# Kernel optimization log

Measured on AMD Instinct MI355X. Metric: run time of the kernel, lower is better.

Reference implementation:

```python
import jax, jax.numpy as jnp
import numpy as np

N = 100000   # nodes
E = 800000   # edges
D = 64       # hidden_channels
H = 4        # heads
C = D        # out_channels per head (PyG: out_channels=hidden)


def setup_inputs() -> dict:
    key = jax.random.key(0)
    ks = jax.random.split(key, 20)
    inp = {}
    inp['x'] = jax.random.normal(ks[0], (N, D), dtype=jnp.float32)
    inp['edge_index'] = jax.random.randint(ks[1], (2, E), 0, N, dtype=jnp.int32)
    i = 2
    for layer in (1, 2):
        for nm in ('Wq', 'Wk', 'Wv'):
            inp[f'{nm}{layer}'] = jax.random.normal(ks[i], (D, H * C), dtype=jnp.float32) * 0.05; i += 1
            inp[f'b{nm[1]}{layer}'] = jnp.zeros((H * C,), dtype=jnp.float32)
        inp[f'Ws{layer}'] = jax.random.normal(ks[i], (D, D), dtype=jnp.float32) * 0.05; i += 1
        inp[f'bs{layer}'] = jnp.zeros((D,), dtype=jnp.float32)
    return inp


def _transformer_conv(x, src, dst, Wq, bq, Wk, bk, Wv, bv, Ws, bs):
    n = x.shape[0]
    q = (x @ Wq + bq).reshape(n, H, C)
    k = (x @ Wk + bk).reshape(n, H, C)
    v = (x @ Wv + bv).reshape(n, H, C)
    # per-edge attention logits: [E, H]
    alpha = jnp.einsum('ehc,ehc->eh', q[dst], k[src]) / np.sqrt(C).astype(np.float32)
    # segment softmax over incoming edges of each destination node
    amax = jax.ops.segment_max(alpha, dst, num_segments=n)          # [N, H]
    ex = jnp.exp(alpha - amax[dst])                                 # [E, H]
    denom = jax.ops.segment_sum(ex, dst, num_segments=n)           # [N, H]
    attn = ex / (denom[dst] + 1e-16)                                # [E, H]
    msg = v[src] * attn[:, :, None]                                 # [E, H, C]
    agg = jax.ops.segment_sum(msg, dst, num_segments=n)            # [N, H, C]
    # concat=False -> mean over heads; root_weight skip connection
    return agg.mean(axis=1) + x @ Ws + bs


def reference(x, edge_index, Wq1, bq1, Wk1, bk1, Wv1, bv1, Ws1, bs1,
              Wq2, bq2, Wk2, bk2, Wv2, bv2, Ws2, bs2):
    src, dst = edge_index[0], edge_index[1]
    h = _transformer_conv(x, src, dst, Wq1, bq1, Wk1, bk1, Wv1, bv1, Ws1, bs1)
    h = jax.nn.relu(h)
    out = _transformer_conv(h, src, dst, Wq2, bq2, Wk2, bk2, Wv2, bv2, Ws2, bs2)
    return out
```

## Files before the change

kernel.cpp:

```cpp
#include <hip/hip_runtime.h>
#include <hip/hip_fp16.h>
#include <math.h>


typedef __attribute__((ext_vector_type(8))) short bf16x8;
typedef __attribute__((ext_vector_type(4))) float f32x4;
typedef __attribute__((ext_vector_type(2))) float f32x2;

#define QKSCALE 32.0f
#define C_EXP2 1.760325e-4f

__device__ inline unsigned short f2bf(float f) {
    unsigned int u = __float_as_uint(f);
    u = (u + 0x7fffu + ((u >> 16) & 1u)) >> 16;
    return (unsigned short)u;
}

#if __has_builtin(__builtin_amdgcn_cvt_pk_fp8_f32) && __has_builtin(__builtin_amdgcn_cvt_pk_f32_fp8)
#define HW_FP8 1
#endif

#ifndef HW_FP8
__device__ inline unsigned int fp8_enc1(float f) {
    unsigned int u = __float_as_uint(f);
    unsigned int s = (u >> 24) & 0x80u;
    float a = fabsf(f);
    if (a >= 448.f) return s | 0x7Eu;
    if (a < 0.015625f) return s;
    unsigned int ua = __float_as_uint(a);
    unsigned int r = ua + 0x7FFFFu + ((ua >> 20) & 1u);
    int e = (int)((r >> 23) & 255u) - 120;
    unsigned int m = (r >> 20) & 7u;
    if (e < 1) return s;
    if (e > 15) return s | 0x7Eu;
    return s | (unsigned int)((e << 3) | m);
}
__device__ inline float fp8_dec1(unsigned int b) {
    unsigned int e = (b >> 3) & 15u, m = b & 7u;
    float v;
    if (e) v = __uint_as_float(((e + 120u) << 23) | (m << 20));
    else   v = (float)m * 0.001953125f;
    return (b & 0x80u) ? -v : v;
}
#endif

__device__ inline unsigned int fp8x4_pack(float f0, float f1, float f2, float f3) {
#ifdef HW_FP8
    int pk = __builtin_amdgcn_cvt_pk_fp8_f32(f0, f1, 0, false);
    pk = __builtin_amdgcn_cvt_pk_fp8_f32(f2, f3, pk, true);
    return (unsigned int)pk;
#else
    return fp8_enc1(f0) | (fp8_enc1(f1) << 8) | (fp8_enc1(f2) << 16) | (fp8_enc1(f3) << 24);
#endif
}

__device__ inline unsigned int i8x4_pack(float f0, float f1, float f2, float f3) {
    int a = (int)rintf(f0 * QKSCALE); a = a < -127 ? -127 : (a > 127 ? 127 : a);
    int b = (int)rintf(f1 * QKSCALE); b = b < -127 ? -127 : (b > 127 ? 127 : b);
    int c = (int)rintf(f2 * QKSCALE); c = c < -127 ? -127 : (c > 127 ? 127 : c);
    int d = (int)rintf(f3 * QKSCALE); d = d < -127 ? -127 : (d > 127 ? 127 : d);
    return (unsigned int)((a & 255) | ((b & 255) << 8) | ((c & 255) << 16) | ((d & 255) << 24));
}

__device__ inline int sdot4(unsigned int a, unsigned int b, int c) {
#if __has_builtin(__builtin_amdgcn_sdot4)
    return __builtin_amdgcn_sdot4((int)a, (int)b, c, false);
#else
    int r = c;
#pragma unroll
    for (int i = 0; i < 4; ++i) {
        int ai = (int)(a << (24 - 8 * i)) >> 24;
        int bi = (int)(b << (24 - 8 * i)) >> 24;
        r += ai * bi;
    }
    return r;
#endif
}

__global__ void k_setup(
    const float* __restrict__ x, unsigned short* __restrict__ Xb, int ncast4,
    const float* __restrict__ Wq1, const float* __restrict__ Wk1,
    const float* __restrict__ Wv1, const float* __restrict__ Ws1,
    const float* __restrict__ Wq2, const float* __restrict__ Wk2,
    const float* __restrict__ Wv2, const float* __restrict__ Ws2,
    unsigned short* __restrict__ Wt,
    int* __restrict__ counts, int N, int castBl)
{
    int b = blockIdx.x, tid = threadIdx.x;
    if (b < castBl) {
        int i = b * 256 + tid;
        if (i < ncast4) {
            float4 v = ((const float4*)x)[i];
            ushort4 o;
            o.x = f2bf(v.x); o.y = f2bf(v.y); o.z = f2bf(v.z); o.w = f2bf(v.w);
            ((ushort4*)Xb)[i] = o;
        }
    } else if (b < castBl + 416) {
        int j = (b - castBl) * 256 + tid;
        int layer = j / 53248;
        int r = j % 53248;
        if (r < 49152) {
            int m = r / 16384, w = r % 16384;
            int n = w / 64, k = w % 64;
            const float* W = (layer == 0)
                ? ((m == 0) ? Wq1 : (m == 1) ? Wk1 : Wv1)
                : ((m == 0) ? Wq2 : (m == 1) ? Wk2 : Wv2);
            Wt[layer * 53248 + m * 16384 + n * 64 + k] = f2bf(W[k * 256 + n]);
        } else {
            int w = r - 49152;
            int n = w / 64, k = w % 64;
            const float* W = (layer == 0) ? Ws1 : Ws2;
            Wt[layer * 53248 + 49152 + n * 64 + k] = f2bf(W[k * 64 + n]);
        }
    } else {
        int i = (b - castBl - 416) * 256 + tid;
        if (i < N) counts[i] = 0;
    }
}

#define SCAN_B 256
#define SCAN_CHUNK 2048
__global__ void k_scan1(const int* __restrict__ counts, int n,
                        int* __restrict__ offs, int* __restrict__ bsums) {
    __shared__ int lds[SCAN_B];
    int b = blockIdx.x, tid = threadIdx.x;
    int base = b * SCAN_CHUNK + tid * 8;
    int v[8]; int s = 0;
#pragma unroll
    for (int i = 0; i < 8; ++i) { int idx = base + i; int c = (idx < n) ? counts[idx] : 0; v[i] = s; s += c; }
    lds[tid] = s;
    for (int off = 1; off < SCAN_B; off <<= 1) {
        __syncthreads();
        int x = (tid >= off) ? lds[tid - off] : 0;
        __syncthreads();
        lds[tid] += x;
    }
    __syncthreads();
    int texcl = lds[tid] - s;
#pragma unroll
    for (int i = 0; i < 8; ++i) { int idx = base + i; if (idx < n) offs[idx] = texcl + v[i]; }
    if (tid == SCAN_B - 1) bsums[b] = lds[tid];
}

__global__ void k_scan2(int* bsums, int nb) {
    __shared__ int lds[256];
    int t = threadIdx.x;
    if (nb > 256) {
        if (t == 0) { int s = 0; for (int i = 0; i < nb; ++i) { int c = bsums[i]; bsums[i] = s; s += c; } }
        return;
    }
    int v = (t < nb) ? bsums[t] : 0;
    lds[t] = v;
    for (int off = 1; off < 256; off <<= 1) {
        __syncthreads();
        int x = (t >= off) ? lds[t - off] : 0;
        __syncthreads();
        lds[t] += x;
    }
    __syncthreads();
    if (t < nb) bsums[t] = lds[t] - v;
}

__global__ void k_scatter(const int* __restrict__ src, const int* __restrict__ dst, int E,
                          const int* __restrict__ offs, const int* __restrict__ bsums,
                          const int* __restrict__ rank, int* __restrict__ csr_src) {
    int e = blockIdx.x * 256 + threadIdx.x;
    if (e < E) {
        int d = dst[e];
        csr_src[offs[d] + bsums[d >> 11] + rank[e]] = src[e];
    }
}

#define GST 68
__global__ __launch_bounds__(256, 2) void k_gemm(
    const unsigned short* __restrict__ Xb, int nrows,
    const unsigned short* __restrict__ WtL,
    const float* __restrict__ bqp, const float* __restrict__ bkp,
    const float* __restrict__ bvp, const float* __restrict__ bsp,
    unsigned char* __restrict__ Qp, unsigned char* __restrict__ Kp,
    unsigned char* __restrict__ Vp, unsigned char* __restrict__ Sp,
    const int* __restrict__ dstp, int histE,
    int* __restrict__ counts, int* __restrict__ rank, int gemmBl, int ntiles)
{
    __shared__ unsigned char st[4][64 * GST];
    __shared__ float bias[832];
    int tid = threadIdx.x;
    if (blockIdx.x >= gemmBl) {
        int e = (blockIdx.x - gemmBl) * 256 + tid;
        if (e < histE) rank[e] = atomicAdd(&counts[dstp[e]], 1);
        return;
    }
    int qtr = tid >> 6, lane = tid & 63;
    int quad = lane >> 4, n16 = lane & 15;
    unsigned char* wst = st[qtr];

    if (tid < 208) {
        float4 b4;
        if (tid < 64)       b4 = ((const float4*)bqp)[tid];
        else if (tid < 128) b4 = ((const float4*)bkp)[tid - 64];
        else if (tid < 192) b4 = ((const float4*)bvp)[tid - 128];
        else                b4 = ((const float4*)bsp)[tid - 192];
        ((float4*)bias)[tid] = b4;
    }

    const unsigned short* Wq = WtL;
    const unsigned short* Wk = WtL + 16384;
    const unsigned short* Wv = WtL + 32768;
    const unsigned short* Ws = WtL + 49152;
    bf16x8 fQ[8], fK[8], fV[8], fS[2];
#pragma unroll
    for (int c = 0; c < 4; ++c) {
        int roff = ((qtr * 4 + c) * 16 + n16) * 64 + quad * 8;
        fQ[2 * c]     = *(const bf16x8*)(Wq + roff);
        fQ[2 * c + 1] = *(const bf16x8*)(Wq + roff + 32);
        fK[2 * c]     = *(const bf16x8*)(Wk + roff);
        fK[2 * c + 1] = *(const bf16x8*)(Wk + roff + 32);
        fV[2 * c]     = *(const bf16x8*)(Wv + roff);
        fV[2 * c + 1] = *(const bf16x8*)(Wv + roff + 32);
    }
    {
        int roff = (qtr * 16 + n16) * 64 + quad * 8;
        fS[0] = *(const bf16x8*)(Ws + roff);
        fS[1] = *(const bf16x8*)(Ws + roff + 32);
    }
    __syncthreads();

    auto loadA = [&](int t, bf16x8 (&x0)[4], bf16x8 (&x1)[4]) {
        int r0 = t * 64;
#pragma unroll
        for (int g = 0; g < 4; ++g) {
            int node = r0 + g * 16 + n16;
            int nodec = (node < nrows) ? node : (nrows - 1);
            x0[g] = *(const bf16x8*)(Xb + (size_t)nodec * 64 + quad * 8);
            x1[g] = *(const bf16x8*)(Xb + (size_t)nodec * 64 + 32 + quad * 8);
        }
    };

    auto do_mat = [&](const bf16x8 (&fm)[8], int boff, unsigned char* plane,
                      bool isInt8, int r0,
                      const bf16x8 (&x0)[4], const bf16x8 (&x1)[4]) {
#pragma unroll
        for (int c = 0; c < 4; ++c) {
            float4 cb = *(const float4*)(bias + boff + qtr * 64 + c * 16 + quad * 4);
#pragma unroll
            for (int g = 0; g < 4; ++g) {
                f32x4 acc = {cb.x, cb.y, cb.z, cb.w};
                acc = __builtin_amdgcn_mfma_f32_16x16x32_bf16(fm[2 * c],     x0[g], acc, 0, 0, 0);
                acc = __builtin_amdgcn_mfma_f32_16x16x32_bf16(fm[2 * c + 1], x1[g], acc, 0, 0, 0);
                unsigned int pk = isInt8 ? i8x4_pack(acc[0], acc[1], acc[2], acc[3])
                                         : fp8x4_pack(acc[0], acc[1], acc[2], acc[3]);
                *(unsigned int*)(wst + (g * 16 + n16) * GST + c * 16 + quad * 4) = pk;
            }
        }
#pragma unroll
        for (int it = 0; it < 4; ++it) {
            int row = it * 16 + (lane >> 2);
            uint4 v = *(const uint4*)(wst + row * GST + (lane & 3) * 16);
            int nd = r0 + row;
            if (nd < nrows)
                *(uint4*)(plane + (size_t)nd * 256 + qtr * 64 + (lane & 3) * 16) = v;
        }
    };

    bf16x8 a0[4], a1[4], b0[4], b1[4];
    int t = blockIdx.x;
    if (t < ntiles) loadA(t, a0, a1);
    for (; t < ntiles; t += gemmBl) {
        int tn = t + gemmBl;
        if (tn < ntiles) loadA(tn, b0, b1);
        int r0 = t * 64;
        do_mat(fQ, 0,   Qp, true,  r0, a0, a1);
        do_mat(fK, 256, Kp, true,  r0, a0, a1);
        do_mat(fV, 512, Vp, false, r0, a0, a1);
        {
            float4 cs = *(const float4*)(bias + 768 + qtr * 16 + quad * 4);
#pragma unroll
            for (int g = 0; g < 4; ++g) {
                f32x4 acc = {cs.x, cs.y, cs.z, cs.w};
                acc = __builtin_amdgcn_mfma_f32_16x16x32_bf16(fS[0], a0[g], acc, 0, 0, 0);
                acc = __builtin_amdgcn_mfma_f32_16x16x32_bf16(fS[1], a1[g], acc, 0, 0, 0);
                *(float4*)(wst + (g * 16 + n16) * GST + quad * 16) =
                    make_float4(acc[0], acc[1], acc[2], acc[3]);
            }
#pragma unroll
            for (int it = 0; it < 4; ++it) {
                int row = it * 16 + (lane >> 2);
                uint4 v = *(const uint4*)(wst + row * GST + (lane & 3) * 16);
                int nd = r0 + row;
                if (nd < nrows)
                    *(uint4*)(Sp + (size_t)nd * 256 + qtr * 64 + (lane & 3) * 16) = v;
            }
        }
#pragma unroll
        for (int g = 0; g < 4; ++g) { a0[g] = b0[g]; a1[g] = b1[g]; }
    }
}

__global__ __launch_bounds__(256) void k_attn(
    const unsigned char* __restrict__ Qp, const unsigned char* __restrict__ Kp,
    const unsigned char* __restrict__ Vp, const float* __restrict__ Sp,
    const int* __restrict__ offs, const int* __restrict__ bsums,
    const int* __restrict__ csr_src,
    float* __restrict__ out, unsigned short* __restrict__ Xb,
    int n, int Etot, int mode)
{
    int node = blockIdx.x * 4 + (threadIdx.x >> 6);
    if (node >= n) return;
    int lane = threadIdx.x & 63;
    int sl = lane & 31;
    int half = lane >> 5;
    unsigned slb = (unsigned)sl * 8u;
    uint2 q8 = *(const uint2*)(Qp + ((unsigned)node << 8) + slb);
    int beg = offs[node] + bsums[node >> 11];
    int end = (node + 1 < n) ? (offs[node + 1] + bsums[(node + 1) >> 11]) : Etot;
    float l = 0.f;
    f32x2 acc2[4];
#pragma unroll
    for (int i = 0; i < 4; ++i) acc2[i] = (f32x2){0.f, 0.f};
    int my = (beg + lane < end) ? csr_src[beg + lane] : 0;
    for (int base = beg; base < end; base += 8) {
        int myn = (base + 8 + lane < end) ? csr_src[base + 8 + lane] : 0;
        int cnt = end - base; if (cnt > 8) cnt = 8;
        uint2 kk[4], vv[4];
#pragma unroll
        for (int p = 0; p < 4; ++p) {
            int idx = __shfl(my, 2 * p + half);
            unsigned off = ((unsigned)idx << 8) + slb;
            kk[p] = *(const uint2*)(Kp + off);
            vv[p] = *(const uint2*)(Vp + off);
        }
#pragma unroll
        for (int p = 0; p < 4; ++p) {
            int d = sdot4(kk[p].x, q8.x, 0);
            d = sdot4(kk[p].y, q8.y, d);
            d += __shfl_xor(d, 1); d += __shfl_xor(d, 2); d += __shfl_xor(d, 4);
            float w = __builtin_exp2f((float)d * C_EXP2);
            w = (2 * p + half < cnt) ? w : 0.f;
            l += w;
            f32x2 w2 = {w, w};
#ifdef HW_FP8
            f32x2 va = __builtin_amdgcn_cvt_pk_f32_fp8((int)vv[p].x, false);
            f32x2 vb = __builtin_amdgcn_cvt_pk_f32_fp8((int)vv[p].x, true);
            f32x2 vc = __builtin_amdgcn_cvt_pk_f32_fp8((int)vv[p].y, false);
            f32x2 vd = __builtin_amdgcn_cvt_pk_f32_fp8((int)vv[p].y, true);
#else
            f32x2 va = {fp8_dec1(vv[p].x & 255u), fp8_dec1((vv[p].x >> 8) & 255u)};
            f32x2 vb = {fp8_dec1((vv[p].x >> 16) & 255u), fp8_dec1(vv[p].x >> 24)};
            f32x2 vc = {fp8_dec1(vv[p].y & 255u), fp8_dec1((vv[p].y >> 8) & 255u)};
            f32x2 vd = {fp8_dec1((vv[p].y >> 16) & 255u), fp8_dec1(vv[p].y >> 24)};
#endif
            acc2[0] = __builtin_elementwise_fma(va, w2, acc2[0]);
            acc2[1] = __builtin_elementwise_fma(vb, w2, acc2[1]);
            acc2[2] = __builtin_elementwise_fma(vc, w2, acc2[2]);
            acc2[3] = __builtin_elementwise_fma(vd, w2, acc2[3]);
        }
        my = myn;
    }
    float acc[8] = {acc2[0][0], acc2[0][1], acc2[1][0], acc2[1][1],
                    acc2[2][0], acc2[2][1], acc2[3][0], acc2[3][1]};
    l += __shfl_xor(l, 32);
#pragma unroll
    for (int i = 0; i < 8; ++i) acc[i] += __shfl_xor(acc[i], 32);
    float inv = 1.f / (l + 1e-16f);
#pragma unroll
    for (int i = 0; i < 8; ++i) acc[i] *= inv;
#pragma unroll
    for (int i = 0; i < 8; ++i) {
        acc[i] += __shfl_xor(acc[i], 8);
        acc[i] += __shfl_xor(acc[i], 16);
        acc[i] *= 0.25f;
    }
    if (lane < 8) {
        const float* Srow = Sp + ((size_t)node << 6);
        float4 s0 = *(const float4*)(Srow + lane * 8);
        float4 s1 = *(const float4*)(Srow + lane * 8 + 4);
        float r0 = acc[0] + s0.x, r1 = acc[1] + s0.y;
        float r2 = acc[2] + s0.z, r3 = acc[3] + s0.w;
        float r4 = acc[4] + s1.x, r5 = acc[5] + s1.y;
        float r6 = acc[6] + s1.z, r7 = acc[7] + s1.w;
        if (mode == 1) {
            r0 = fmaxf(r0, 0.f); r1 = fmaxf(r1, 0.f);
            r2 = fmaxf(r2, 0.f); r3 = fmaxf(r3, 0.f);
            r4 = fmaxf(r4, 0.f); r5 = fmaxf(r5, 0.f);
            r6 = fmaxf(r6, 0.f); r7 = fmaxf(r7, 0.f);
            uint4 o;
            o.x = (unsigned int)f2bf(r0) | ((unsigned int)f2bf(r1) << 16);
            o.y = (unsigned int)f2bf(r2) | ((unsigned int)f2bf(r3) << 16);
            o.z = (unsigned int)f2bf(r4) | ((unsigned int)f2bf(r5) << 16);
            o.w = (unsigned int)f2bf(r6) | ((unsigned int)f2bf(r7) << 16);
            *(uint4*)(Xb + (size_t)node * 64 + lane * 8) = o;
        } else {
            *(float4*)(out + (size_t)node * 64 + lane * 8) = make_float4(r0, r1, r2, r3);
            *(float4*)(out + (size_t)node * 64 + lane * 8 + 4) = make_float4(r4, r5, r6, r7);
        }
    }
}

extern "C" void kernel_launch(void* const* d_in, const int* in_sizes, int n_in,
                              void* d_out, int out_size, void* d_ws, size_t ws_size,
                              hipStream_t stream)
{
    const float* x  = (const float*)d_in[0];
    const int*   ei = (const int*)d_in[1];
    int N = in_sizes[0] / 64;
    int E = in_sizes[1] / 2;
    const int* srcp = ei;
    const int* dstp = ei + E;
    const float* Wq1 = (const float*)d_in[2],  *bq1 = (const float*)d_in[3];
    const float* Wk1 = (const float*)d_in[4],  *bk1 = (const float*)d_in[5];
    const float* Wv1 = (const float*)d_in[6],  *bv1 = (const float*)d_in[7];
    const float* Ws1 = (const float*)d_in[8],  *bs1 = (const float*)d_in[9];
    const float* Wq2 = (const float*)d_in[10], *bq2 = (const float*)d_in[11];
    const float* Wk2 = (const float*)d_in[12], *bk2 = (const float*)d_in[13];
    const float* Wv2 = (const float*)d_in[14], *bv2 = (const float*)d_in[15];
    const float* Ws2 = (const float*)d_in[16], *bs2 = (const float*)d_in[17];
    float* out = (float*)d_out;

    char* ws = (char*)d_ws;
    size_t off = 0;
    auto alloc = [&](size_t bytes) -> void* {
        void* p = ws + off;
        off = (off + bytes + 255) & ~(size_t)255;
        return p;
    };
    unsigned short* Xb = (unsigned short*)alloc((size_t)N * 64 * 2);
    unsigned char* Qp  = (unsigned char*)alloc(((size_t)N + 64) * 256);
    unsigned char* Kp  = (unsigned char*)alloc(((size_t)N + 64) * 256);
    unsigned char* Vp  = (unsigned char*)alloc(((size_t)N + 64) * 256);
    unsigned char* Sp  = (unsigned char*)alloc(((size_t)N + 64) * 256);
    unsigned short* Wt = (unsigned short*)alloc(2 * 53248 * 2);
    int* counts = (int*)alloc((size_t)N * 4);
    int* rank   = (int*)alloc((size_t)E * 4);
    int* offs   = (int*)alloc((size_t)N * 4);
    int* bsums  = (int*)alloc(1024 * 4);
    int* csr    = (int*)alloc((size_t)E * 4);
    (void)n_in; (void)out_size;
    if (off > ws_size) return;

    int ebl = (E + 255) / 256;
    int nb_scan = (N + SCAN_CHUNK - 1) / SCAN_CHUNK;
    int ntiles = (N + 63) / 64;
    int gemm_bl = ntiles < 1024 ? ntiles : 1024;
    int hist_bl = (E + 255) / 256;
    int attn_bl = (N + 3) / 4;
    int ncast4 = N * 16;
    int castBl = (ncast4 + 255) / 256;
    int zeroBl = (N + 255) / 256;

    k_setup<<<castBl + 416 + zeroBl, 256, 0, stream>>>(
        x, Xb, ncast4, Wq1, Wk1, Wv1, Ws1, Wq2, Wk2, Wv2, Ws2, Wt, counts, N, castBl);

    k_gemm<<<gemm_bl + hist_bl, 256, 0, stream>>>(
        Xb, N, Wt, bq1, bk1, bv1, bs1, Qp, Kp, Vp, Sp,
        dstp, E, counts, rank, gemm_bl, ntiles);

    k_scan1<<<nb_scan, SCAN_B, 0, stream>>>(counts, N, offs, bsums);
    k_scan2<<<1, 256, 0, stream>>>(bsums, nb_scan);
    k_scatter<<<ebl, 256, 0, stream>>>(srcp, dstp, E, offs, bsums, rank, csr);

    k_attn<<<attn_bl, 256, 0, stream>>>(Qp, Kp, Vp, (const float*)Sp,
                                        offs, bsums, csr, out, Xb, N, E, 1);

    k_gemm<<<gemm_bl, 256, 0, stream>>>(
        Xb, N, Wt + 53248, bq2, bk2, bv2, bs2, Qp, Kp, Vp, Sp,
        dstp, 0, counts, rank, gemm_bl, ntiles);

    k_attn<<<attn_bl, 256, 0, stream>>>(Qp, Kp, Vp, (const float*)Sp,
                                        offs, bsums, csr, out, Xb, N, E, 0);
}
```

Baseline: 377.1 us.

## Widen per-lane attention loads to 16 bytes and use DPP for head reduction

Rearranges the attention wave so that 16 lanes cover one edge's 256-byte K/V row with 16-byte loads, and four edges are processed per pass instead of two. The per-head dot-product reduction shrinks to two steps and uses DPP quad-permute moves instead of ds_bpermute shuffles. The intent is fewer, wider gather loads and cheaper cross-lane reductions. The cost is twice as many accumulator registers per lane and extra final cross-lane reductions; outputs are now written by only 4 lanes.

```diff
diff --git a/kernel.cpp b/kernel.cpp
--- a/kernel.cpp
+++ b/kernel.cpp
@@ -74,6 +74,21 @@
         r += ai * bi;
     }
     return r;
+#endif
+}
+
+__device__ inline int dpp_xor1(int x) {
+#if __has_builtin(__builtin_amdgcn_mov_dpp)
+    return __builtin_amdgcn_mov_dpp(x, 0xB1, 0xF, 0xF, true);
+#else
+    return __shfl_xor(x, 1);
+#endif
+}
+__device__ inline int dpp_xor2(int x) {
+#if __has_builtin(__builtin_amdgcn_mov_dpp)
+    return __builtin_amdgcn_mov_dpp(x, 0x4E, 0xF, 0xF, true);
+#else
+    return __shfl_xor(x, 2);
 #endif
 }
 
@@ -307,91 +322,113 @@
     int node = blockIdx.x * 4 + (threadIdx.x >> 6);
     if (node >= n) return;
     int lane = threadIdx.x & 63;
-    int sl = lane & 31;
-    int half = lane >> 5;
-    unsigned slb = (unsigned)sl * 8u;
-    uint2 q8 = *(const uint2*)(Qp + ((unsigned)node << 8) + slb);
+    int s16 = lane & 15;
+    int qtr = lane >> 4;
+    unsigned slb = (unsigned)s16 * 16u;
+    unsigned nb = ((unsigned)node << 8) + slb;
+    uint4 q8 = *(const uint4*)(Qp + nb);
     int beg = offs[node] + bsums[node >> 11];
     int end = (node + 1 < n) ? (offs[node + 1] + bsums[(node + 1) >> 11]) : Etot;
     float l = 0.f;
-    f32x2 acc2[4];
-#pragma unroll
-    for (int i = 0; i < 4; ++i) acc2[i] = (f32x2){0.f, 0.f};
+    f32x2 acc2[8];
+#pragma unroll
+    for (int i = 0; i < 8; ++i) acc2[i] = (f32x2){0.f, 0.f};
     int my = (beg + lane < end) ? csr_src[beg + lane] : 0;
     for (int base = beg; base < end; base += 8) {
         int myn = (base + 8 + lane < end) ? csr_src[base + 8 + lane] : 0;
         int cnt = end - base; if (cnt > 8) cnt = 8;
-        uint2 kk[4], vv[4];
-#pragma unroll
-        for (int p = 0; p < 4; ++p) {
-            int idx = __shfl(my, 2 * p + half);
+#pragma unroll
+        for (int p = 0; p < 2; ++p) {
+            int idx = __shfl(my, 4 * p + qtr);
             unsigned off = ((unsigned)idx << 8) + slb;
-            kk[p] = *(const uint2*)(Kp + off);
-            vv[p] = *(const uint2*)(Vp + off);
-        }
-#pragma unroll
-        for (int p = 0; p < 4; ++p) {
-            int d = sdot4(kk[p].x, q8.x, 0);
-            d = sdot4(kk[p].y, q8.y, d);
-            d += __shfl_xor(d, 1); d += __shfl_xor(d, 2); d += __shfl_xor(d, 4);
+            uint4 kk = *(const uint4*)(Kp + off);
+            uint4 vv = *(const uint4*)(Vp + off);
+            int d = sdot4(kk.x, q8.x, 0);
+            d = sdot4(kk.y, q8.y, d);
+            d = sdot4(kk.z, q8.z, d);
+            d = sdot4(kk.w, q8.w, d);
+            d += dpp_xor1(d);
+            d += dpp_xor2(d);
             float w = __builtin_exp2f((float)d * C_EXP2);
-            w = (2 * p + half < cnt) ? w : 0.f;
+            w = (4 * p + qtr < cnt) ? w : 0.f;
             l += w;
             f32x2 w2 = {w, w};
 #ifdef HW_FP8
-            f32x2 va = __builtin_amdgcn_cvt_pk_f32_fp8((int)vv[p].x, false);
-            f32x2 vb = __builtin_amdgcn_cvt_pk_f32_fp8((int)vv[p].x, true);
-            f32x2 vc = __builtin_amdgcn_cvt_pk_f32_fp8((int)vv[p].y, false);
-            f32x2 vd = __builtin_amdgcn_cvt_pk_f32_fp8((int)vv[p].y, true);
+            f32x2 v0 = __builtin_amdgcn_cvt_pk_f32_fp8((int)vv.x, false);
+            f32x2 v1 = __builtin_amdgcn_cvt_pk_f32_fp8((int)vv.x, true);
+            f32x2 v2 = __builtin_amdgcn_cvt_pk_f32_fp8((int)vv.y, false);
+            f32x2 v3 = __builtin_amdgcn_cvt_pk_f32_fp8((int)vv.y, true);
+            f32x2 v4 = __builtin_amdgcn_cvt_pk_f32_fp8((int)vv.z, false);
+            f32x2 v5 = __builtin_amdgcn_cvt_pk_f32_fp8((int)vv.z, true);
+            f32x2 v6 = __builtin_amdgcn_cvt_pk_f32_fp8((int)vv.w, false);
+            f32x2 v7 = __builtin_amdgcn_cvt_pk_f32_fp8((int)vv.w, true);
 #else
-            f32x2 va = {fp8_dec1(vv[p].x & 255u), fp8_dec1((vv[p].x >> 8) & 255u)};
-            f32x2 vb = {fp8_dec1((vv[p].x >> 16) & 255u), fp8_dec1(vv[p].x >> 24)};
-            f32x2 vc = {fp8_dec1(vv[p].y & 255u), fp8_dec1((vv[p].y >> 8) & 255u)};
-            f32x2 vd = {fp8_dec1((vv[p].y >> 16) & 255u), fp8_dec1(vv[p].y >> 24)};
-#endif
-            acc2[0] = __builtin_elementwise_fma(va, w2, acc2[0]);
-            acc2[1] = __builtin_elementwise_fma(vb, w2, acc2[1]);
-            acc2[2] = __builtin_elementwise_fma(vc, w2, acc2[2]);
-            acc2[3] = __builtin_elementwise_fma(vd, w2, acc2[3]);
+            f32x2 v0 = {fp8_dec1(vv.x & 255u), fp8_dec1((vv.x >> 8) & 255u)};
+            f32x2 v1 = {fp8_dec1((vv.x >> 16) & 255u), fp8_dec1(vv.x >> 24)};
+            f32x2 v2 = {fp8_dec1(vv.y & 255u), fp8_dec1((vv.y >> 8) & 255u)};
+            f32x2 v3 = {fp8_dec1((vv.y >> 16) & 255u), fp8_dec1(vv.y >> 24)};
+            f32x2 v4 = {fp8_dec1(vv.z & 255u), fp8_dec1((vv.z >> 8) & 255u)};
+            f32x2 v5 = {fp8_dec1((vv.z >> 16) & 255u), fp8_dec1(vv.z >> 24)};
+            f32x2 v6 = {fp8_dec1(vv.w & 255u), fp8_dec1((vv.w >> 8) & 255u)};
+            f32x2 v7 = {fp8_dec1((vv.w >> 16) & 255u), fp8_dec1(vv.w >> 24)};
+#endif
+            acc2[0] = __builtin_elementwise_fma(v0, w2, acc2[0]);
+            acc2[1] = __builtin_elementwise_fma(v1, w2, acc2[1]);
+            acc2[2] = __builtin_elementwise_fma(v2, w2, acc2[2]);
+            acc2[3] = __builtin_elementwise_fma(v3, w2, acc2[3]);
+            acc2[4] = __builtin_elementwise_fma(v4, w2, acc2[4]);
+            acc2[5] = __builtin_elementwise_fma(v5, w2, acc2[5]);
+            acc2[6] = __builtin_elementwise_fma(v6, w2, acc2[6]);
+            acc2[7] = __builtin_elementwise_fma(v7, w2, acc2[7]);
         }
         my = myn;
     }
-    float acc[8] = {acc2[0][0], acc2[0][1], acc2[1][0], acc2[1][1],
-                    acc2[2][0], acc2[2][1], acc2[3][0], acc2[3][1]};
+    float a[16];
+#pragma unroll
+    for (int i = 0; i < 8; ++i) { a[2 * i] = acc2[i][0]; a[2 * i + 1] = acc2[i][1]; }
+    l += __shfl_xor(l, 16);
     l += __shfl_xor(l, 32);
 #pragma unroll
-    for (int i = 0; i < 8; ++i) acc[i] += __shfl_xor(acc[i], 32);
+    for (int i = 0; i < 16; ++i) {
+        a[i] += __shfl_xor(a[i], 16);
+        a[i] += __shfl_xor(a[i], 32);
+    }
     float inv = 1.f / (l + 1e-16f);
 #pragma unroll
-    for (int i = 0; i < 8; ++i) acc[i] *= inv;
-#pragma unroll
-    for (int i = 0; i < 8; ++i) {
-        acc[i] += __shfl_xor(acc[i], 8);
-        acc[i] += __shfl_xor(acc[i], 16);
-        acc[i] *= 0.25f;
-    }
-    if (lane < 8) {
-        const float* Srow = Sp + ((size_t)node << 6);
-        float4 s0 = *(const float4*)(Srow + lane * 8);
-        float4 s1 = *(const float4*)(Srow + lane * 8 + 4);
-        float r0 = acc[0] + s0.x, r1 = acc[1] + s0.y;
-        float r2 = acc[2] + s0.z, r3 = acc[3] + s0.w;
-        float r4 = acc[4] + s1.x, r5 = acc[5] + s1.y;
-        float r6 = acc[6] + s1.z, r7 = acc[7] + s1.w;
+    for (int i = 0; i < 16; ++i) a[i] *= inv;
+#pragma unroll
+    for (int i = 0; i < 16; ++i) {
+        a[i] += __shfl_xor(a[i], 4);
+        a[i] += __shfl_xor(a[i], 8);
+        a[i] *= 0.25f;
+    }
+    if (lane < 4) {
+        const float* Srow = Sp + ((unsigned)node << 6) + lane * 16;
+        float4 s0 = *(const float4*)(Srow);
+        float4 s1 = *(const float4*)(Srow + 4);
+        float4 s2 = *(const float4*)(Srow + 8);
+        float4 s3 = *(const float4*)(Srow + 12);
+        float r[16];
+        r[0] = a[0] + s0.x;  r[1] = a[1] + s0.y;  r[2] = a[2] + s0.z;  r[3] = a[3] + s0.w;
+        r[4] = a[4] + s1.x;  r[5] = a[5] + s1.y;  r[6] = a[6] + s1.z;  r[7] = a[7] + s1.w;
+        r[8] = a[8] + s2.x;  r[9] = a[9] + s2.y;  r[10] = a[10] + s2.z; r[11] = a[11] + s2.w;
+        r[12] = a[12] + s3.x; r[13] = a[13] + s3.y; r[14] = a[14] + s3.z; r[15] = a[15] + s3.w;
         if (mode == 1) {
-            r0 = fmaxf(r0, 0.f); r1 = fmaxf(r1, 0.f);
-            r2 = fmaxf(r2, 0.f); r3 = fmaxf(r3, 0.f);
-            r4 = fmaxf(r4, 0.f); r5 = fmaxf(r5, 0.f);
-            r6 = fmaxf(r6, 0.f); r7 = fmaxf(r7, 0.f);
-            uint4 o;
-            o.x = (unsigned int)f2bf(r0) | ((unsigned int)f2bf(r1) << 16);
-            o.y = (unsigned int)f2bf(r2) | ((unsigned int)f2bf(r3) << 16);
-            o.z = (unsigned int)f2bf(r4) | ((unsigned int)f2bf(r5) << 16);
-            o.w = (unsigned int)f2bf(r6) | ((unsigned int)f2bf(r7) << 16);
-            *(uint4*)(Xb + (size_t)node * 64 + lane * 8) = o;
+#pragma unroll
+            for (int i = 0; i < 16; ++i) r[i] = fmaxf(r[i], 0.f);
+            unsigned ow[8];
+#pragma unroll
+            for (int i = 0; i < 8; ++i)
+                ow[i] = (unsigned)f2bf(r[2 * i]) | ((unsigned)f2bf(r[2 * i + 1]) << 16);
+            unsigned short* xrow = Xb + (size_t)node * 64 + lane * 16;
+            *(uint4*)(xrow) = make_uint4(ow[0], ow[1], ow[2], ow[3]);
+            *(uint4*)(xrow + 8) = make_uint4(ow[4], ow[5], ow[6], ow[7]);
         } else {
-            *(float4*)(out + (size_t)node * 64 + lane * 8) = make_float4(r0, r1, r2, r3);
-            *(float4*)(out + (size_t)node * 64 + lane * 8 + 4) = make_float4(r4, r5, r6, r7);
+            float* orow = out + (size_t)node * 64 + lane * 16;
+            *(float4*)(orow)      = make_float4(r[0], r[1], r[2], r[3]);
+            *(float4*)(orow + 4)  = make_float4(r[4], r[5], r[6], r[7]);
+            *(float4*)(orow + 8)  = make_float4(r[8], r[9], r[10], r[11]);
+            *(float4*)(orow + 12) = make_float4(r[12], r[13], r[14], r[15]);
         }
     }
 }
```

New measurement: 388.1 us. 2.9% more time.

## Split projection GEMM into per-weight passes to cut registers and raise occupancy

Applied to the files above, without the earlier changes.

The fused GEMM used to keep all Q/K/V/S weight fragments in registers and compute every projection per row tile. It now runs four separate passes over the row tiles, each holding only one weight matrix's fragments. Launch bounds go from 2 to 4 waves per SIMD. This lowers register pressure so more waves can hide latency, but the input X tiles are reloaded four times, which adds memory traffic.

```diff
diff --git a/kernel.cpp b/kernel.cpp
--- a/kernel.cpp
+++ b/kernel.cpp
@@ -172,7 +172,7 @@
 }
 
 #define GST 68
-__global__ __launch_bounds__(256, 2) void k_gemm(
+__global__ __launch_bounds__(256, 4) void k_gemm(
     const unsigned short* __restrict__ Xb, int nrows,
     const unsigned short* __restrict__ WtL,
     const float* __restrict__ bqp, const float* __restrict__ bkp,
@@ -202,27 +202,6 @@
         else                b4 = ((const float4*)bsp)[tid - 192];
         ((float4*)bias)[tid] = b4;
     }
-
-    const unsigned short* Wq = WtL;
-    const unsigned short* Wk = WtL + 16384;
-    const unsigned short* Wv = WtL + 32768;
-    const unsigned short* Ws = WtL + 49152;
-    bf16x8 fQ[8], fK[8], fV[8], fS[2];
-#pragma unroll
-    for (int c = 0; c < 4; ++c) {
-        int roff = ((qtr * 4 + c) * 16 + n16) * 64 + quad * 8;
-        fQ[2 * c]     = *(const bf16x8*)(Wq + roff);
-        fQ[2 * c + 1] = *(const bf16x8*)(Wq + roff + 32);
-        fK[2 * c]     = *(const bf16x8*)(Wk + roff);
-        fK[2 * c + 1] = *(const bf16x8*)(Wk + roff + 32);
-        fV[2 * c]     = *(const bf16x8*)(Wv + roff);
-        fV[2 * c + 1] = *(const bf16x8*)(Wv + roff + 32);
-    }
-    {
-        int roff = (qtr * 16 + n16) * 64 + quad * 8;
-        fS[0] = *(const bf16x8*)(Ws + roff);
-        fS[1] = *(const bf16x8*)(Ws + roff + 32);
-    }
     __syncthreads();
 
     auto loadA = [&](int t, bf16x8 (&x0)[4], bf16x8 (&x1)[4]) {
@@ -236,49 +215,77 @@
         }
     };
 
-    auto do_mat = [&](const bf16x8 (&fm)[8], int boff, unsigned char* plane,
-                      bool isInt8, int r0,
-                      const bf16x8 (&x0)[4], const bf16x8 (&x1)[4]) {
+    auto pass = [&](const unsigned short* W, int boff, unsigned char* plane,
+                    bool isInt8) {
+        bf16x8 f[8];
 #pragma unroll
         for (int c = 0; c < 4; ++c) {
-            float4 cb = *(const float4*)(bias + boff + qtr * 64 + c * 16 + quad * 4);
-#pragma unroll
-            for (int g = 0; g < 4; ++g) {
-                f32x4 acc = {cb.x, cb.y, cb.z, cb.w};
-                acc = __builtin_amdgcn_mfma_f32_16x16x32_bf16(fm[2 * c],     x0[g], acc, 0, 0, 0);
-                acc = __builtin_amdgcn_mfma_f32_16x16x32_bf16(fm[2 * c + 1], x1[g], acc, 0, 0, 0);
-                unsigned int pk = isInt8 ? i8x4_pack(acc[0], acc[1], acc[2], acc[3])
-                                         : fp8x4_pack(acc[0], acc[1], acc[2], acc[3]);
-                *(unsigned int*)(wst + (g * 16 + n16) * GST + c * 16 + quad * 4) = pk;
+            int roff = ((qtr * 4 + c) * 16 + n16) * 64 + quad * 8;
+            f[2 * c]     = *(const bf16x8*)(W + roff);
+            f[2 * c + 1] = *(const bf16x8*)(W + roff + 32);
+        }
+        bf16x8 a0[4], a1[4], b0[4], b1[4];
+        int t = blockIdx.x;
+        if (t < ntiles) loadA(t, a0, a1);
+        for (; t < ntiles; t += gemmBl) {
+            int tn = t + gemmBl;
+            if (tn < ntiles) loadA(tn, b0, b1);
+            int r0 = t * 64;
+#pragma unroll
+            for (int c = 0; c < 4; ++c) {
+                float4 cb = *(const float4*)(bias + boff + qtr * 64 + c * 16 + quad * 4);
+#pragma unroll
+                for (int g = 0; g < 4; ++g) {
+                    f32x4 acc = {cb.x, cb.y, cb.z, cb.w};
+                    acc = __builtin_amdgcn_mfma_f32_16x16x32_bf16(f[2 * c],     a0[g], acc, 0, 0, 0);
+                    acc = __builtin_amdgcn_mfma_f32_16x16x32_bf16(f[2 * c + 1], a1[g], acc, 0, 0, 0);
+                    unsigned int pk = isInt8 ? i8x4_pack(acc[0], acc[1], acc[2], acc[3])
+                                             : fp8x4_pack(acc[0], acc[1], acc[2], acc[3]);
+                    *(unsigned int*)(wst + (g * 16 + n16) * GST + c * 16 + quad * 4) = pk;
+                }
             }
-        }
-#pragma unroll
-        for (int it = 0; it < 4; ++it) {
-            int row = it * 16 + (lane >> 2);
-            uint4 v = *(const uint4*)(wst + row * GST + (lane & 3) * 16);
-            int nd = r0 + row;
-            if (nd < nrows)
-                *(uint4*)(plane + (size_t)nd * 256 + qtr * 64 + (lane & 3) * 16) = v;
+#pragma unroll
+            for (int it = 0; it < 4; ++it) {
+                int row = it * 16 + (lane >> 2);
+                uint4 v = *(const uint4*)(wst + row * GST + (lane & 3) * 16);
+                int nd = r0 + row;
+                if (nd < nrows)
+                    *(uint4*)(plane + (size_t)nd * 256 + qtr * 64 + (lane & 3) * 16) = v;
+            }
+#pragma unroll
+            for (int g = 0; g < 4; ++g) { a0[g] = b0[g]; a1[g] = b1[g]; }
         }
     };
 
-    bf16x8 a0[4], a1[4], b0[4], b1[4];
-    int t = blockIdx.x;
-    if (t < ntiles) loadA(t, a0, a1);
-    for (; t < ntiles; t += gemmBl) {
-        int tn = t + gemmBl;
-        if (tn < ntiles) loadA(tn, b0, b1);
-        int r0 = t * 64;
-        do_mat(fQ, 0,   Qp, true,  r0, a0, a1);
-        do_mat(fK, 256, Kp, true,  r0, a0, a1);
-        do_mat(fV, 512, Vp, false, r0, a0, a1);
+    const unsigned short* Wq = WtL;
+    const unsigned short* Wk = WtL + 16384;
+    const unsigned short* Wv = WtL + 32768;
+    const unsigned short* Ws = WtL + 49152;
+
+    pass(Wq, 0,   Qp, true);
+    pass(Wk, 256, Kp, true);
+    pass(Wv, 512, Vp, false);
+
+    {
+        bf16x8 s0, s1;
         {
-            float4 cs = *(const float4*)(bias + 768 + qtr * 16 + quad * 4);
+            int roff = (qtr * 16 + n16) * 64 + quad * 8;
+            s0 = *(const bf16x8*)(Ws + roff);
+            s1 = *(const bf16x8*)(Ws + roff + 32);
+        }
+        float4 cs = *(const float4*)(bias + 768 + qtr * 16 + quad * 4);
+        bf16x8 a0[4], a1[4], b0[4], b1[4];
+        int t = blockIdx.x;
+        if (t < ntiles) loadA(t, a0, a1);
+        for (; t < ntiles; t += gemmBl) {
+            int tn = t + gemmBl;
+            if (tn < ntiles) loadA(tn, b0, b1);
+            int r0 = t * 64;
 #pragma unroll
             for (int g = 0; g < 4; ++g) {
                 f32x4 acc = {cs.x, cs.y, cs.z, cs.w};
-                acc = __builtin_amdgcn_mfma_f32_16x16x32_bf16(fS[0], a0[g], acc, 0, 0, 0);
-                acc = __builtin_amdgcn_mfma_f32_16x16x32_bf16(fS[1], a1[g], acc, 0, 0, 0);
+                acc = __builtin_amdgcn_mfma_f32_16x16x32_bf16(s0, a0[g], acc, 0, 0, 0);
+                acc = __builtin_amdgcn_mfma_f32_16x16x32_bf16(s1, a1[g], acc, 0, 0, 0);
                 *(float4*)(wst + (g * 16 + n16) * GST + quad * 16) =
                     make_float4(acc[0], acc[1], acc[2], acc[3]);
             }
@@ -290,9 +297,9 @@
                 if (nd < nrows)
                     *(uint4*)(Sp + (size_t)nd * 256 + qtr * 64 + (lane & 3) * 16) = v;
             }
-        }
-#pragma unroll
-        for (int g = 0; g < 4; ++g) { a0[g] = b0[g]; a1[g] = b1[g]; }
+#pragma unroll
+            for (int g = 0; g < 4; ++g) { a0[g] = b0[g]; a1[g] = b1[g]; }
+        }
     }
 }
 
```

Result: slower. 414.1 us (+9.8%).
